# Performance work log

Hardware: AMD Instinct MI355X
Metric: run time of the kernel (lower is better)

The kernel has to match this reference:

```python
import jax, jax.numpy as jnp
import numpy as np

R = 48          # n_comp (== n_comp_xy)
X = Y = Z = 300 # world_size
C = 27          # channels
N = 1_000_000   # query points
XYZ_MIN = 0.0
XYZ_MAX = 1.0


def _sample2d(plane, gh, gw):
    """Bilinear grid_sample, align_corners=True.
    plane: [R, H, W]; gh, gw: [N] normalized coords in [-1, 1] indexing H and W.
    Returns [N, R].
    """
    H, W = plane.shape[1], plane.shape[2]
    ih = (gh + 1.0) * 0.5 * (H - 1)
    iw = (gw + 1.0) * 0.5 * (W - 1)
    i0 = jnp.clip(jnp.floor(ih).astype(jnp.int32), 0, H - 1)
    j0 = jnp.clip(jnp.floor(iw).astype(jnp.int32), 0, W - 1)
    i1 = jnp.minimum(i0 + 1, H - 1)
    j1 = jnp.minimum(j0 + 1, W - 1)
    fh = (ih - i0.astype(ih.dtype))[:, None]  # [N,1]
    fw = (iw - j0.astype(iw.dtype))[:, None]
    p00 = plane[:, i0, j0].T  # [N,R]
    p01 = plane[:, i0, j1].T
    p10 = plane[:, i1, j0].T
    p11 = plane[:, i1, j1].T
    top = p00 * (1 - fw) + p01 * fw
    bot = p10 * (1 - fw) + p11 * fw
    return top * (1 - fh) + bot * fh


def _sample1d(vec, g):
    """Linear interp along length dim (width of the [*,*,L,1] torch vec is 1,
    sampled at 0 -> pure 1D interp).  vec: [R, L]; g: [N] in [-1,1] -> [N,R]."""
    L = vec.shape[1]
    ih = (g + 1.0) * 0.5 * (L - 1)
    i0 = jnp.clip(jnp.floor(ih).astype(jnp.int32), 0, L - 1)
    i1 = jnp.minimum(i0 + 1, L - 1)
    f = (ih - i0.astype(ih.dtype))[:, None]
    return vec[:, i0].T * (1 - f) + vec[:, i1].T * f


def setup_inputs() -> dict:
    key = jax.random.key(0)
    ks = jax.random.split(key, 8)
    return {
        "xyz": jax.random.uniform(ks[0], (N, 3), dtype=jnp.float32),
        "xy_plane": jax.random.normal(ks[1], (R, X, Y), dtype=jnp.float32) * 0.1,
        "xz_plane": jax.random.normal(ks[2], (R, X, Z), dtype=jnp.float32) * 0.1,
        "yz_plane": jax.random.normal(ks[3], (R, Y, Z), dtype=jnp.float32) * 0.1,
        "x_vec": jax.random.normal(ks[4], (R, X), dtype=jnp.float32) * 0.1,
        "y_vec": jax.random.normal(ks[5], (R, Y), dtype=jnp.float32) * 0.1,
        "z_vec": jax.random.normal(ks[6], (R, Z), dtype=jnp.float32) * 0.1,
        "f_vec": jax.random.uniform(ks[7], (3 * R, C), dtype=jnp.float32,
                                     minval=-0.1, maxval=0.1),
    }


def reference(xyz, xy_plane, xz_plane, yz_plane, x_vec, y_vec, z_vec, f_vec):
    # normalize to [-1, 1]
    g = (xyz - XYZ_MIN) / (XYZ_MAX - XYZ_MIN) * 2.0 - 1.0  # [N,3]
    gx, gy, gz = g[:, 0], g[:, 1], g[:, 2]
    xy_feat = _sample2d(xy_plane, gx, gy)  # [N,R]
    xz_feat = _sample2d(xz_plane, gx, gz)
    yz_feat = _sample2d(yz_plane, gy, gz)
    x_feat = _sample1d(x_vec, gx)
    y_feat = _sample1d(y_vec, gy)
    z_feat = _sample1d(z_vec, gz)
    feat = jnp.concatenate([xy_feat * z_feat, xz_feat * y_feat, yz_feat * x_feat],
                           axis=-1)  # [N, 3R]
    return feat @ f_vec  # [N, C]
```

## Files before the change

kernel.cpp:

```cpp
#include <hip/hip_runtime.h>

#define RR 48
#define GG 300
#define HW2 (GG * GG)
#define NPLANE (RR * HW2)
#define NVEC (RR * GG)
#define CC 27
#define NBUCK 32768
#define TP 64
#define TPP 65

#define TROWS 16
#define TCOLS 256
#define PCHUNK ((HW2 + TCOLS - 1) / TCOLS)
#define NPASS (RR / TROWS)
#define TPB3 (3 * NPASS * PCHUNK)
#define VBLK ((3 * NVEC + 255) / 256)
#define TROW2 260

struct Axis { int i0, i1; float f; };

__device__ __forceinline__ Axis axis_interp(float x) {
  float g = x * 2.0f - 1.0f;
  float ih = (g + 1.0f) * 0.5f * (float)(GG - 1);
  int i0 = (int)floorf(ih);
  i0 = i0 < 0 ? 0 : (i0 > GG - 1 ? GG - 1 : i0);
  int i1 = i0 + 1 > GG - 1 ? GG - 1 : i0 + 1;
  Axis a; a.i0 = i0; a.i1 = i1; a.f = ih - (float)i0;
  return a;
}

__device__ __forceinline__ unsigned part3(unsigned v) {
  unsigned r = 0;
  r |= (v & 1u);
  r |= (v & 2u) << 2;
  r |= (v & 4u) << 4;
  r |= (v & 8u) << 6;
  r |= (v & 16u) << 8;
  return r;
}

__device__ __forceinline__ int morton_key(float x, float y, float z) {
  int qx = (int)(x * 32.0f); qx = qx < 0 ? 0 : (qx > 31 ? 31 : qx);
  int qy = (int)(y * 32.0f); qy = qy < 0 ? 0 : (qy > 31 ? 31 : qy);
  int qz = (int)(z * 32.0f); qz = qz < 0 ? 0 : (qz > 31 ? 31 : qz);
  return (int)(part3((unsigned)qx) | (part3((unsigned)qy) << 1) | (part3((unsigned)qz) << 2));
}

__global__ void __launch_bounds__(256) hist_kernel(const float* __restrict__ xyz, int n,
                                                   int* __restrict__ offs) {
  int i = blockIdx.x * blockDim.x + threadIdx.x;
  if (i >= n) return;
  atomicAdd(&offs[morton_key(xyz[i * 3], xyz[i * 3 + 1], xyz[i * 3 + 2])], 1);
}

__global__ void __launch_bounds__(1024) scan_kernel(int* __restrict__ offs) {
  __shared__ int part[1024];
  int t = threadIdx.x;
  int base = t * (NBUCK / 1024);
  int loc[NBUCK / 1024];
  int s = 0;
#pragma unroll
  for (int i = 0; i < NBUCK / 1024; ++i) { loc[i] = offs[base + i]; s += loc[i]; }
  part[t] = s;
  __syncthreads();
  for (int off = 1; off < 1024; off <<= 1) {
    int u = (t >= off) ? part[t - off] : 0;
    __syncthreads();
    part[t] += u;
    __syncthreads();
  }
  int excl = (t == 0) ? 0 : part[t - 1];
#pragma unroll
  for (int i = 0; i < NBUCK / 1024; ++i) {
    int c = loc[i];
    offs[base + i] = excl;
    excl += c;
  }
}

__global__ void __launch_bounds__(256) trans_scatter_kernel(
    const float* __restrict__ xyz, int n, int* __restrict__ offs,
    int* __restrict__ sidx, float4* __restrict__ sxyz, int scb,
    const float* __restrict__ p0, const float* __restrict__ p1, const float* __restrict__ p2,
    float* __restrict__ t0, float* __restrict__ t1, float* __restrict__ t2,
    const float* __restrict__ v0, const float* __restrict__ v1, const float* __restrict__ v2,
    float* __restrict__ tv0, float* __restrict__ tv1, float* __restrict__ tv2) {
  __shared__ float tile[TROWS * TROW2];
  int bb = blockIdx.x;
  int t = threadIdx.x;

  if (bb < scb) {
    int i = bb * 256 + t;
    if (i < n) {
      float x = xyz[i * 3], y = xyz[i * 3 + 1], z = xyz[i * 3 + 2];
      int key = morton_key(x, y, z);
      int pos = atomicAdd(&offs[key], 1);
      if (sxyz) sxyz[pos] = make_float4(x, y, z, __int_as_float(i));
      else      sidx[pos] = i;
    }
  } else if (bb < scb + TPB3) {
    int rem = bb - scb;
    int plane = rem / (NPASS * PCHUNK);
    rem -= plane * (NPASS * PCHUNK);
    int pass = rem / PCHUNK;
    int chunk = rem - pass * PCHUNK;
    const float* in = (plane == 0) ? p0 : (plane == 1) ? p1 : p2;
    float* outp = (plane == 0) ? t0 : (plane == 1) ? t1 : t2;
    int base = chunk * TCOLS;
    int rbase = pass * TROWS;

    int p4 = t & 63;
    int rg = t >> 6;
#pragma unroll
    for (int i = 0; i < TROWS / 4; ++i) {
      int r = i * 4 + rg;
      int pos = base + p4 * 4;
      if (pos < HW2) {
        float4 v = *(const float4*)(in + (size_t)(rbase + r) * HW2 + pos);
        *(float4*)&tile[r * TROW2 + p4 * 4] = v;
      }
    }
    __syncthreads();

    int c4 = t & 3;
    int hwl = t >> 2;
#pragma unroll
    for (int jj = 0; jj < 4; ++jj) {
      int hw = jj * 64 + hwl;
      if (base + hw < HW2) {
        float4 w;
        w.x = tile[(c4 * 4 + 0) * TROW2 + hw];
        w.y = tile[(c4 * 4 + 1) * TROW2 + hw];
        w.z = tile[(c4 * 4 + 2) * TROW2 + hw];
        w.w = tile[(c4 * 4 + 3) * TROW2 + hw];
        *(float4*)(outp + (size_t)(base + hw) * RR + rbase + c4 * 4) = w;
      }
    }
  } else {
    int e = (bb - scb - TPB3) * 256 + t;
    if (e < 3 * NVEC) {
      int v = e / NVEC;
      int rem = e - v * NVEC;
      int i = rem / RR;
      int r = rem - i * RR;
      const float* in = (v == 0) ? v0 : (v == 1) ? v1 : v2;
      float* out = (v == 0) ? tv0 : (v == 1) ? tv1 : tv2;
      out[i * RR + r] = in[r * GG + i];
    }
  }
}

__device__ __forceinline__ void gather_seg(const float* __restrict__ P, Axis ai, Axis aj,
                                           const float* __restrict__ V, Axis ak,
                                           int r4, float* __restrict__ dst) {
  float fi = ai.f, fj = aj.f, fk = ak.f;
  float w00 = (1.f - fi) * (1.f - fj);
  float w01 = (1.f - fi) * fj;
  float w10 = fi * (1.f - fj);
  float w11 = fi * fj;
  float omk = 1.f - fk;
  float4 q00 = *(const float4*)(P + (ai.i0 * GG + aj.i0) * RR + r4);
  float4 q01 = *(const float4*)(P + (ai.i0 * GG + aj.i1) * RR + r4);
  float4 q10 = *(const float4*)(P + (ai.i1 * GG + aj.i0) * RR + r4);
  float4 q11 = *(const float4*)(P + (ai.i1 * GG + aj.i1) * RR + r4);
  float4 b0 = *(const float4*)(V + ak.i0 * RR + r4);
  float4 b1 = *(const float4*)(V + ak.i1 * RR + r4);
  float t0 = (w00 * q00.x + w01 * q01.x + w10 * q10.x + w11 * q11.x) * (omk * b0.x + fk * b1.x);
  float t1 = (w00 * q00.y + w01 * q01.y + w10 * q10.y + w11 * q11.y) * (omk * b0.y + fk * b1.y);
  float t2 = (w00 * q00.z + w01 * q01.z + w10 * q10.z + w11 * q11.z) * (omk * b0.z + fk * b1.z);
  float t3 = (w00 * q00.w + w01 * q01.w + w10 * q10.w + w11 * q11.w) * (omk * b0.w + fk * b1.w);
  dst[(r4 + 0) * TPP] = t0;
  dst[(r4 + 1) * TPP] = t1;
  dst[(r4 + 2) * TPP] = t2;
  dst[(r4 + 3) * TPP] = t3;
}

__global__ void __launch_bounds__(256, 4) tensorf_fused(
    const float4* __restrict__ sxyz, const int* __restrict__ sidx,
    const float* __restrict__ xyz,
    const float* __restrict__ Txy, const float* __restrict__ Txz, const float* __restrict__ Tyz,
    const float* __restrict__ Tx, const float* __restrict__ Ty, const float* __restrict__ Tz,
    const float* __restrict__ F, float* __restrict__ out, int n, int chunkLen) {
  __shared__ float featT[144 * TPP];
  __shared__ int oiS[TP];
  int b = blockIdx.x;
  int nb = (b & 7) * chunkLen + (b >> 3);
  int base = nb * TP;
  int tid = threadIdx.x;
  int g = tid >> 4;
  int l = tid & 15;

#pragma unroll 1
  for (int it = 0; it < TP / 16; ++it) {
    int pl = (it << 4) + g;
    int sp = base + pl;
    if (sp < n) {
      float x, y, z;
      int oi;
      if (sxyz) {
        float4 p4 = sxyz[sp];
        x = p4.x; y = p4.y; z = p4.z;
        oi = __float_as_int(p4.w);
      } else {
        oi = sidx[sp];
        x = xyz[oi * 3 + 0];
        y = xyz[oi * 3 + 1];
        z = xyz[oi * 3 + 2];
      }
      if (l == 12) oiS[pl] = oi;
      Axis ax = axis_interp(x), ay = axis_interp(y), az = axis_interp(z);
      if (l < 12) {
        int r4 = l << 2;
        float* dst = &featT[pl];
        gather_seg(Txy, ax, ay, Tz, az, r4, dst + 0 * RR * TPP);
        gather_seg(Txz, ax, az, Ty, ay, r4, dst + 1 * RR * TPP);
        gather_seg(Tyz, ay, az, Tx, ax, r4, dst + 2 * RR * TPP);
      }
    }
  }
  __syncthreads();

  int p = tid & (TP - 1);
  int q = __builtin_amdgcn_readfirstlane(tid >> 6);
  int cbase = (q == 3) ? 20 : q * 7;
  const float* Fh = F + cbase;

  float acc[7];
#pragma unroll
  for (int c = 0; c < 7; ++c) acc[c] = 0.f;

#pragma unroll 4
  for (int k = 0; k < 144; ++k) {
    float fv = featT[k * TPP + p];
#pragma unroll
    for (int c = 0; c < 7; ++c) acc[c] = fmaf(fv, Fh[k * CC + c], acc[c]);
  }

  int sp = base + p;
  if (sp < n) {
    int oi = oiS[p];
    float* o = out + (size_t)oi * CC + cbase;
    if (q != 3) o[0] = acc[0];
#pragma unroll
    for (int c = 1; c < 7; ++c) o[c] = acc[c];
  }
}

__global__ void __launch_bounds__(256) tensorf_naive(
    const float* __restrict__ xyz,
    const float* __restrict__ Pxy, const float* __restrict__ Pxz, const float* __restrict__ Pyz,
    const float* __restrict__ Vx, const float* __restrict__ Vy, const float* __restrict__ Vz,
    const float* __restrict__ F, float* __restrict__ out, int n) {
  int idx = blockIdx.x * blockDim.x + threadIdx.x;
  if (idx >= n) return;
  float x = xyz[idx * 3], y = xyz[idx * 3 + 1], z = xyz[idx * 3 + 2];
  Axis ax = axis_interp(x), ay = axis_interp(y), az = axis_interp(z);
  float acc[CC];
#pragma unroll
  for (int c = 0; c < CC; ++c) acc[c] = 0.f;
  const float* Ps[3] = {Pxy, Pxz, Pyz};
  const float* Vs[3] = {Vz, Vy, Vx};
  Axis A[3][2] = {{ax, ay}, {ax, az}, {ay, az}};
  Axis K[3] = {az, ay, ax};
#pragma unroll 1
  for (int s = 0; s < 3; ++s) {
    Axis ai = A[s][0], aj = A[s][1], ak = K[s];
    float fi = ai.f, fj = aj.f, fk = ak.f;
    float w00 = (1.f - fi) * (1.f - fj), w01 = (1.f - fi) * fj;
    float w10 = fi * (1.f - fj), w11 = fi * fj, omk = 1.f - fk;
#pragma unroll 1
    for (int r = 0; r < RR; ++r) {
      const float* pr = Ps[s] + r * HW2;
      float ft = (w00 * pr[ai.i0 * GG + aj.i0] + w01 * pr[ai.i0 * GG + aj.i1] +
                  w10 * pr[ai.i1 * GG + aj.i0] + w11 * pr[ai.i1 * GG + aj.i1]) *
                 (omk * Vs[s][r * GG + ak.i0] + fk * Vs[s][r * GG + ak.i1]);
      const float* Fr = F + (s * RR + r) * CC;
#pragma unroll
      for (int c = 0; c < CC; ++c) acc[c] = fmaf(ft, Fr[c], acc[c]);
    }
  }
  float* o = out + (size_t)idx * CC;
#pragma unroll
  for (int c = 0; c < CC; ++c) o[c] = acc[c];
}

extern "C" void kernel_launch(void* const* d_in, const int* in_sizes, int n_in,
                              void* d_out, int out_size, void* d_ws, size_t ws_size,
                              hipStream_t stream) {
  const float* xyz = (const float*)d_in[0];
  const float* pxy = (const float*)d_in[1];
  const float* pxz = (const float*)d_in[2];
  const float* pyz = (const float*)d_in[3];
  const float* vx = (const float*)d_in[4];
  const float* vy = (const float*)d_in[5];
  const float* vz = (const float*)d_in[6];
  const float* F = (const float*)d_in[7];
  float* out = (float*)d_out;
  int n = in_sizes[0] / 3;
  int nblk = (n + 255) / 256;

  size_t fixed = (size_t)(3 * NPLANE + 3 * NVEC) * sizeof(float) +
                 (size_t)NBUCK * sizeof(int);
  size_t need1 = fixed + (size_t)n * sizeof(int);
  size_t need2 = fixed + (size_t)n * sizeof(float4);

  if (ws_size >= need1) {
    float* w = (float*)d_ws;
    float* Txy = w;
    float* Txz = Txy + NPLANE;
    float* Tyz = Txz + NPLANE;
    float* Tx = Tyz + NPLANE;
    float* Ty = Tx + NVEC;
    float* Tz = Ty + NVEC;
    int* offs = (int*)(Tz + NVEC);

    int* sidx = nullptr;
    float4* sxyz = nullptr;
    if (ws_size >= need2) sxyz = (float4*)(offs + NBUCK);
    else sidx = (int*)(offs + NBUCK);

    hipMemsetAsync(offs, 0, (size_t)NBUCK * sizeof(int), stream);
    hist_kernel<<<nblk, 256, 0, stream>>>(xyz, n, offs);
    scan_kernel<<<1, 1024, 0, stream>>>(offs);
    trans_scatter_kernel<<<nblk + TPB3 + VBLK, 256, 0, stream>>>(
        xyz, n, offs, sidx, sxyz, nblk,
        pxy, pxz, pyz, Txy, Txz, Tyz, vx, vy, vz, Tx, Ty, Tz);

    int ntile = (n + TP - 1) / TP;
    int chunkLen = (ntile + 7) / 8;
    tensorf_fused<<<chunkLen * 8, 256, 0, stream>>>(sxyz, sidx, xyz, Txy, Txz, Tyz,
                                                    Tx, Ty, Tz, F, out, n, chunkLen);
  } else {
    tensorf_naive<<<nblk, 256, 0, stream>>>(xyz, pxy, pxz, pyz, vx, vy, vz, F, out, n);
  }
}
```

Baseline: 544.2 us.

## Merge histogram, scan, scatter and transposes into one cooperative kernel

```diff
diff --git a/kernel.cpp b/kernel.cpp
--- a/kernel.cpp
+++ b/kernel.cpp
@@ -1,4 +1,7 @@
 #include <hip/hip_runtime.h>
+#include <hip/hip_cooperative_groups.h>
+
+namespace cg = cooperative_groups;
 
 #define RR 48
 #define GG 300
@@ -17,6 +20,7 @@
 #define TPB3 (3 * NPASS * PCHUNK)
 #define VBLK ((3 * NVEC + 255) / 256)
 #define TROW2 260
+#define SCANB (NBUCK / 256)
 
 struct Axis { int i0, i1; float f; };
 
@@ -45,6 +49,136 @@
   int qy = (int)(y * 32.0f); qy = qy < 0 ? 0 : (qy > 31 ? 31 : qy);
   int qz = (int)(z * 32.0f); qz = qz < 0 ? 0 : (qz > 31 ? 31 : qz);
   return (int)(part3((unsigned)qx) | (part3((unsigned)qy) << 1) | (part3((unsigned)qz) << 2));
+}
+
+__device__ __forceinline__ void plane_transpose_vb(
+    int vb, int t, float* __restrict__ tile,
+    const float* __restrict__ p0, const float* __restrict__ p1, const float* __restrict__ p2,
+    float* __restrict__ t0, float* __restrict__ t1, float* __restrict__ t2) {
+  int rem = vb;
+  int plane = rem / (NPASS * PCHUNK);
+  rem -= plane * (NPASS * PCHUNK);
+  int pass = rem / PCHUNK;
+  int chunk = rem - pass * PCHUNK;
+  const float* in = (plane == 0) ? p0 : (plane == 1) ? p1 : p2;
+  float* outp = (plane == 0) ? t0 : (plane == 1) ? t1 : t2;
+  int base = chunk * TCOLS;
+  int rbase = pass * TROWS;
+
+  int p4 = t & 63;
+  int rg = t >> 6;
+#pragma unroll
+  for (int i = 0; i < TROWS / 4; ++i) {
+    int r = i * 4 + rg;
+    int pos = base + p4 * 4;
+    if (pos < HW2) {
+      float4 v = *(const float4*)(in + (size_t)(rbase + r) * HW2 + pos);
+      *(float4*)&tile[r * TROW2 + p4 * 4] = v;
+    }
+  }
+  __syncthreads();
+
+  int c4 = t & 3;
+  int hwl = t >> 2;
+#pragma unroll
+  for (int jj = 0; jj < 4; ++jj) {
+    int hw = jj * 64 + hwl;
+    if (base + hw < HW2) {
+      float4 w;
+      w.x = tile[(c4 * 4 + 0) * TROW2 + hw];
+      w.y = tile[(c4 * 4 + 1) * TROW2 + hw];
+      w.z = tile[(c4 * 4 + 2) * TROW2 + hw];
+      w.w = tile[(c4 * 4 + 3) * TROW2 + hw];
+      *(float4*)(outp + (size_t)(base + hw) * RR + rbase + c4 * 4) = w;
+    }
+  }
+}
+
+__device__ __forceinline__ void vec_transpose_e(
+    int e, const float* __restrict__ v0, const float* __restrict__ v1,
+    const float* __restrict__ v2, float* __restrict__ tv0,
+    float* __restrict__ tv1, float* __restrict__ tv2) {
+  if (e < 3 * NVEC) {
+    int v = e / NVEC;
+    int rem = e - v * NVEC;
+    int i = rem / RR;
+    int r = rem - i * RR;
+    const float* in = (v == 0) ? v0 : (v == 1) ? v1 : v2;
+    float* out = (v == 0) ? tv0 : (v == 1) ? tv1 : tv2;
+    out[i * RR + r] = in[r * GG + i];
+  }
+}
+
+__global__ void __launch_bounds__(256) preprocess_coop(
+    const float* __restrict__ xyz, int n,
+    int* __restrict__ offs, int* __restrict__ aux,
+    int* __restrict__ sidx, float4* __restrict__ sxyz,
+    const float* __restrict__ p0, const float* __restrict__ p1, const float* __restrict__ p2,
+    float* __restrict__ t0, float* __restrict__ t1, float* __restrict__ t2,
+    const float* __restrict__ v0, const float* __restrict__ v1, const float* __restrict__ v2,
+    float* __restrict__ tv0, float* __restrict__ tv1, float* __restrict__ tv2) {
+  cg::grid_group grid = cg::this_grid();
+  __shared__ float tile[TROWS * TROW2];
+  int* itile = (int*)tile;
+  int t = threadIdx.x;
+  int gtid = blockIdx.x * 256 + t;
+  int gsize = gridDim.x * 256;
+
+  int nvbA = TPB3 + VBLK + (n + 255) / 256;
+  for (int vb = blockIdx.x; vb < nvbA; vb += gridDim.x) {
+    __syncthreads();
+    if (vb < TPB3) {
+      plane_transpose_vb(vb, t, tile, p0, p1, p2, t0, t1, t2);
+    } else if (vb < TPB3 + VBLK) {
+      vec_transpose_e((vb - TPB3) * 256 + t, v0, v1, v2, tv0, tv1, tv2);
+    } else {
+      int i = (vb - TPB3 - VBLK) * 256 + t;
+      if (i < n)
+        atomicAdd(&offs[morton_key(xyz[i * 3], xyz[i * 3 + 1], xyz[i * 3 + 2])], 1);
+    }
+  }
+  grid.sync();
+
+  int cnt = 0;
+  if (blockIdx.x < SCANB) {
+    cnt = offs[gtid];
+    itile[t] = cnt;
+    __syncthreads();
+    for (int off = 1; off < 256; off <<= 1) {
+      int u = (t >= off) ? itile[t - off] : 0;
+      __syncthreads();
+      itile[t] += u;
+      __syncthreads();
+    }
+    offs[gtid] = itile[t] - cnt;
+    if (t == 255) aux[blockIdx.x] = itile[t];
+  }
+  grid.sync();
+
+  if (blockIdx.x == 0) {
+    int v = (t < SCANB) ? aux[t] : 0;
+    itile[t] = v;
+    __syncthreads();
+    for (int off = 1; off < 256; off <<= 1) {
+      int u = (t >= off) ? itile[t - off] : 0;
+      __syncthreads();
+      itile[t] += u;
+      __syncthreads();
+    }
+    if (t < SCANB) aux[t] = itile[t] - v;
+  }
+  grid.sync();
+
+  if (blockIdx.x < SCANB) offs[gtid] += aux[blockIdx.x];
+  grid.sync();
+
+  for (int i = gtid; i < n; i += gsize) {
+    float x = xyz[i * 3], y = xyz[i * 3 + 1], z = xyz[i * 3 + 2];
+    int key = morton_key(x, y, z);
+    int pos = atomicAdd(&offs[key], 1);
+    if (sxyz) sxyz[pos] = make_float4(x, y, z, __int_as_float(i));
+    else      sidx[pos] = i;
+  }
 }
 
 __global__ void __launch_bounds__(256) hist_kernel(const float* __restrict__ xyz, int n,
@@ -100,54 +234,9 @@
       else      sidx[pos] = i;
     }
   } else if (bb < scb + TPB3) {
-    int rem = bb - scb;
-    int plane = rem / (NPASS * PCHUNK);
-    rem -= plane * (NPASS * PCHUNK);
-    int pass = rem / PCHUNK;
-    int chunk = rem - pass * PCHUNK;
-    const float* in = (plane == 0) ? p0 : (plane == 1) ? p1 : p2;
-    float* outp = (plane == 0) ? t0 : (plane == 1) ? t1 : t2;
-    int base = chunk * TCOLS;
-    int rbase = pass * TROWS;
-
-    int p4 = t & 63;
-    int rg = t >> 6;
-#pragma unroll
-    for (int i = 0; i < TROWS / 4; ++i) {
-      int r = i * 4 + rg;
-      int pos = base + p4 * 4;
-      if (pos < HW2) {
-        float4 v = *(const float4*)(in + (size_t)(rbase + r) * HW2 + pos);
-        *(float4*)&tile[r * TROW2 + p4 * 4] = v;
-      }
-    }
-    __syncthreads();
-
-    int c4 = t & 3;
-    int hwl = t >> 2;
-#pragma unroll
-    for (int jj = 0; jj < 4; ++jj) {
-      int hw = jj * 64 + hwl;
-      if (base + hw < HW2) {
-        float4 w;
-        w.x = tile[(c4 * 4 + 0) * TROW2 + hw];
-        w.y = tile[(c4 * 4 + 1) * TROW2 + hw];
-        w.z = tile[(c4 * 4 + 2) * TROW2 + hw];
-        w.w = tile[(c4 * 4 + 3) * TROW2 + hw];
-        *(float4*)(outp + (size_t)(base + hw) * RR + rbase + c4 * 4) = w;
-      }
-    }
+    plane_transpose_vb(bb - scb, t, tile, p0, p1, p2, t0, t1, t2);
   } else {
-    int e = (bb - scb - TPB3) * 256 + t;
-    if (e < 3 * NVEC) {
-      int v = e / NVEC;
-      int rem = e - v * NVEC;
-      int i = rem / RR;
-      int r = rem - i * RR;
-      const float* in = (v == 0) ? v0 : (v == 1) ? v1 : v2;
-      float* out = (v == 0) ? tv0 : (v == 1) ? tv1 : tv2;
-      out[i * RR + r] = in[r * GG + i];
-    }
+    vec_transpose_e((bb - scb - TPB3) * 256 + t, v0, v1, v2, tv0, tv1, tv2);
   }
 }
 
@@ -301,7 +390,7 @@
   int nblk = (n + 255) / 256;
 
   size_t fixed = (size_t)(3 * NPLANE + 3 * NVEC) * sizeof(float) +
-                 (size_t)NBUCK * sizeof(int);
+                 (size_t)(NBUCK + 256) * sizeof(int);
   size_t need1 = fixed + (size_t)n * sizeof(int);
   size_t need2 = fixed + (size_t)n * sizeof(float4);
 
@@ -314,18 +403,49 @@
     float* Ty = Tx + NVEC;
     float* Tz = Ty + NVEC;
     int* offs = (int*)(Tz + NVEC);
+    int* aux = offs + NBUCK;
 
     int* sidx = nullptr;
     float4* sxyz = nullptr;
-    if (ws_size >= need2) sxyz = (float4*)(offs + NBUCK);
-    else sidx = (int*)(offs + NBUCK);
+    if (ws_size >= need2) sxyz = (float4*)(aux + 256);
+    else sidx = aux + 256;
 
     hipMemsetAsync(offs, 0, (size_t)NBUCK * sizeof(int), stream);
-    hist_kernel<<<nblk, 256, 0, stream>>>(xyz, n, offs);
-    scan_kernel<<<1, 1024, 0, stream>>>(offs);
-    trans_scatter_kernel<<<nblk + TPB3 + VBLK, 256, 0, stream>>>(
-        xyz, n, offs, sidx, sxyz, nblk,
-        pxy, pxz, pyz, Txy, Txz, Tyz, vx, vy, vz, Tx, Ty, Tz);
+
+    static int coopGrid = -1;
+    if (coopGrid < 0) {
+      int bpc = 0, dev = 0;
+      hipDeviceProp_t prop;
+      if (hipOccupancyMaxActiveBlocksPerMultiprocessor(&bpc, preprocess_coop, 256, 0) ==
+              hipSuccess &&
+          bpc > 0 && hipGetDevice(&dev) == hipSuccess &&
+          hipGetDeviceProperties(&prop, dev) == hipSuccess) {
+        long g = (long)bpc * prop.multiProcessorCount;
+        coopGrid = (int)(g > 4096 ? 4096 : g);
+      } else {
+        coopGrid = 0;
+      }
+    }
+
+    bool coopOK = false;
+    if (coopGrid >= SCANB) {
+      void* args[] = {(void*)&xyz, (void*)&n,   (void*)&offs, (void*)&aux,
+                      (void*)&sidx, (void*)&sxyz, (void*)&pxy,  (void*)&pxz,
+                      (void*)&pyz,  (void*)&Txy,  (void*)&Txz,  (void*)&Tyz,
+                      (void*)&vx,   (void*)&vy,   (void*)&vz,   (void*)&Tx,
+                      (void*)&Ty,   (void*)&Tz};
+      hipError_t e = hipLaunchCooperativeKernel((const void*)preprocess_coop,
+                                                dim3(coopGrid), dim3(256), args, 0, stream);
+      coopOK = (e == hipSuccess);
+    }
+
+    if (!coopOK) {
+      hist_kernel<<<nblk, 256, 0, stream>>>(xyz, n, offs);
+      scan_kernel<<<1, 1024, 0, stream>>>(offs);
+      trans_scatter_kernel<<<nblk + TPB3 + VBLK, 256, 0, stream>>>(
+          xyz, n, offs, sidx, sxyz, nblk,
+          pxy, pxz, pyz, Txy, Txz, Tyz, vx, vy, vz, Tx, Ty, Tz);
+    }
 
     int ntile = (n + TP - 1) / TP;
     int chunkLen = (ntile + 7) / 8;
```

Result: slower. 1.097 ms (+101.5%).
